# Kernel optimization log

Hardware: AMD Instinct MI355X
Metric: run time of the kernel (lower is better)

The kernel has to match this reference:

```python
import jax, jax.numpy as jnp
import numpy as np

B, T, IN, D = 32, 1024, 1536, 768


def setup_inputs() -> dict:
    key = jax.random.key(0)
    ks = jax.random.split(key, 14)
    s_in = 1.0 / np.sqrt(IN)
    s_d = 1.0 / np.sqrt(D)
    return {
        "x": jax.random.normal(ks[0], (B, T, IN), jnp.float32),
        # fc1/fc2 torch Linear weights stored [out, in]
        "fc1_w": jax.random.normal(ks[1], (IN, IN), jnp.float32) * s_in,
        "fc1_b": jax.random.normal(ks[2], (IN,), jnp.float32) * 0.01,
        "fc2_w": jax.random.normal(ks[3], (D, IN), jnp.float32) * s_in,
        "fc2_b": jax.random.normal(ks[4], (D,), jnp.float32) * 0.01,
        # Unary: Conv1d(D,D,k=1) then Conv1d(D,1,k=1); k=1 conv == per-token linear
        "un_emb_w": jax.random.normal(ks[5], (D, D), jnp.float32) * s_d,
        "un_emb_b": jax.random.normal(ks[6], (D,), jnp.float32) * 0.01,
        "un_red_w": jax.random.normal(ks[7], (1, D), jnp.float32) * s_d,
        "un_red_b": jax.random.normal(ks[8], (1,), jnp.float32) * 0.01,
        # Self Pairwise: x_embedding / y_embedding Conv1d(D,D,k=1)
        "pw_x_w": jax.random.normal(ks[9], (D, D), jnp.float32) * s_d,
        "pw_x_b": jax.random.normal(ks[10], (D,), jnp.float32) * 0.01,
        "pw_y_w": jax.random.normal(ks[11], (D, D), jnp.float32) * s_d,
        "pw_y_b": jax.random.normal(ks[12], (D,), jnp.float32) * 0.01,
        # reduce_potentials: Conv1d(2,1,k=1,bias=False) -> 2 scalars
        "red_w": jax.random.normal(ks[13], (2,), jnp.float32),
    }


def reference(x, fc1_w, fc1_b, fc2_w, fc2_b,
              un_emb_w, un_emb_b, un_red_w, un_red_b,
              pw_x_w, pw_x_b, pw_y_w, pw_y_b, red_w):
    # FGAEmbedder MLP: fc2(relu(fc1(x)))
    h = jax.nn.relu(jnp.einsum('bti,oi->bto', x, fc1_w) + fc1_b)
    u = jnp.einsum('bti,oi->bto', h, fc2_w) + fc2_b            # [B,T,D]

    # Unary potential (dropout is identity at inference)
    e = jax.nn.relu(jnp.einsum('btd,od->bto', u, un_emb_w) + un_emb_b)
    un_pot = (jnp.einsum('btd,od->bto', e, un_red_w) + un_red_b)[..., 0]  # [B,T]

    # Self pairwise: cosine-similarity matrix, marginalized by mean (spatial_dim=None)
    xe = jnp.einsum('btd,od->bto', u, pw_x_w) + pw_x_b
    ye = jnp.einsum('btd,od->bto', u, pw_y_w) + pw_y_b
    xn = xe / jnp.maximum(jnp.linalg.norm(xe, axis=-1, keepdims=True), 1e-12)
    yn = ye / jnp.maximum(jnp.linalg.norm(ye, axis=-1, keepdims=True), 1e-12)
    S = jnp.einsum('btd,bsd->bts', xn, yn)                     # [B,T,T]
    pw_pot = jnp.mean(S, axis=2)                               # [B,T]

    # reduce potentials (Conv1d 2->1 no bias; order: unary then self), softmax attention
    scores = red_w[0] * un_pot + red_w[1] * pw_pot             # [B,T]
    w = jax.nn.softmax(scores, axis=1)
    return jnp.einsum('btd,bt->bd', u, w)                      # [B,D]
```

## Files before the change

kernel.cpp:

```cpp
#include <hip/hip_runtime.h>
#include <stdint.h>

#define MROWS 32768
#define TSEQ  1024
#define BBATCH 32
#define INDIM 1536
#define DDIM  768
#define NCAT  2304

typedef short short8 __attribute__((ext_vector_type(8)));
typedef short short4v __attribute__((ext_vector_type(4)));
typedef float f32x4  __attribute__((ext_vector_type(4)));

__device__ __forceinline__ float b2f(ushort u) {
    union { uint32_t u; float f; } x; x.u = ((uint32_t)u) << 16; return x.f;
}
__device__ __forceinline__ ushort f2b(float f) {
    union { float f; uint32_t u; } x; x.f = f;
    uint32_t r = x.u + 0x7fffu + ((x.u >> 16) & 1u);
    return (ushort)(r >> 16);
}

__device__ __forceinline__ void cvt4(const float* __restrict__ in, ushort* __restrict__ out, int i) {
    float4 v = ((const float4*)in)[i];
    ushort4 o;
    o.x = f2b(v.x); o.y = f2b(v.y); o.z = f2b(v.z); o.w = f2b(v.w);
    ((ushort4*)out)[i] = o;
}

#define C0 12582912
#define C1 13172736
#define C2 13467648
#define C3 13615104
#define C4 13762560
#define C5 13910016
#define C6 13910592
#define C7 13916736
#define C8 13922880
#define C9 13947456
__global__ void cvt_all(const float* __restrict__ x,
                        const float* __restrict__ fc1_w, const float* __restrict__ fc2_w,
                        const float* __restrict__ w3a, const float* __restrict__ w3b,
                        const float* __restrict__ w3c,
                        const float* __restrict__ ba, const float* __restrict__ bb,
                        const float* __restrict__ bc,
                        ushort* __restrict__ X16, ushort* __restrict__ W1,
                        ushort* __restrict__ W2, ushort* __restrict__ W3,
                        float* __restrict__ B3, float* __restrict__ ybar_z,
                        float* __restrict__ out_z, float* __restrict__ stats_z)
{
    int i = blockIdx.x * 256 + threadIdx.x;
    float4 z = {0.f, 0.f, 0.f, 0.f};
    if (i < C0)       cvt4(x, X16, i);
    else if (i < C1)  cvt4(fc1_w, W1, i - C0);
    else if (i < C2)  cvt4(fc2_w, W2, i - C1);
    else if (i < C3)  cvt4(w3a, W3,           i - C2);
    else if (i < C4)  cvt4(w3b, W3 + 589824,  i - C3);
    else if (i < C5)  cvt4(w3c, W3 + 1179648, i - C4);
    else if (i < C6) {
        int j = i - C5;
        const float* src = (j < 192) ? ba : (j < 384) ? bb : bc;
        int off = (j < 192) ? j : (j < 384) ? (j - 192) : (j - 384);
        ((float4*)B3)[j] = ((const float4*)src)[off];
    }
    else if (i < C7)  ((float4*)ybar_z)[i - C6] = z;
    else if (i < C8)  ((float4*)out_z)[i - C7] = z;
    else if (i < C9)  ((float4*)stats_z)[i - C8] = z;
}

__global__ __launch_bounds__(256, 2)
void gemm_bt(const ushort* __restrict__ A, const ushort* __restrict__ Bm,
             const float* __restrict__ bias, ushort* __restrict__ C,
             int M, int N, int K, int relu_ncols,
             const float* __restrict__ urw, float* __restrict__ SE,
             float* __restrict__ SX, float* __restrict__ SY)
{
    __shared__ __align__(16) ushort lA[128 * 64];
    __shared__ __align__(16) ushort lB[128 * 64];

    const int tid  = threadIdx.x;
    const int lane = tid & 63, wave = tid >> 6;
    const int wm = wave & 1, wn = wave >> 1;
    const int quad = lane >> 4, r16 = lane & 15;

    const int ntiles = N >> 7;
    const int xcd = blockIdx.x & 7;
    const int j   = blockIdx.x >> 3;
    const int g   = j / ntiles;
    const int n_t = j - g * ntiles;
    const int m_t = xcd + (g << 3);
    const int m0 = m_t * 128, n0 = n_t * 128;

    const int srow = lane >> 2;
    const int scol = ((lane & 3) ^ ((lane >> 3) & 3)) * 8;
    const int goff = (r16 << 5) + ((quad ^ ((r16 >> 1) & 3)) << 3);

    f32x4 acc[4][4] = {};

    const int kIters = K >> 6;
    for (int kt = 0; kt < kIters; ++kt) {
        const int k0 = kt << 6;
        __syncthreads();
#pragma unroll
        for (int c = 0; c < 4; ++c) {
            int S  = wave * 4 + c;
            int kh = S >> 3, rs = S & 7;
            int row = rs * 16 + srow;
            int kc  = k0 + kh * 32 + scol;
            const ushort* ga = A + (size_t)(m0 + row) * K + kc;
            __builtin_amdgcn_global_load_lds(
                (const __attribute__((address_space(1))) void*)ga,
                (__attribute__((address_space(3))) void*)&lA[S * 512], 16, 0, 0);
            const ushort* gb = Bm + (size_t)(n0 + row) * K + kc;
            __builtin_amdgcn_global_load_lds(
                (const __attribute__((address_space(1))) void*)gb,
                (__attribute__((address_space(3))) void*)&lB[S * 512], 16, 0, 0);
        }
        __syncthreads();

#pragma unroll
        for (int kh = 0; kh < 2; ++kh) {
            short8 af[4], bf[4];
#pragma unroll
            for (int i = 0; i < 4; ++i)
                af[i] = *(const short8*)&lA[kh * 4096 + (wm * 4 + i) * 512 + goff];
#pragma unroll
            for (int j2 = 0; j2 < 4; ++j2)
                bf[j2] = *(const short8*)&lB[kh * 4096 + (wn * 4 + j2) * 512 + goff];
#pragma unroll
            for (int i = 0; i < 4; ++i)
#pragma unroll
                for (int j2 = 0; j2 < 4; ++j2)
                    acc[i][j2] = __builtin_amdgcn_mfma_f32_16x16x32_bf16(af[i], bf[j2], acc[i][j2], 0, 0, 0);
        }
    }

    const bool stats = (urw != nullptr);
    const int sec = n0 / DDIM;
    float st[4][4] = {};
#pragma unroll
    for (int j2 = 0; j2 < 4; ++j2) {
        int gn = n0 + wn * 64 + j2 * 16 + r16;
        float bv = bias[gn];
        bool dorelu = gn < relu_ncols;
        float uw = (stats && sec == 0) ? urw[gn] : 0.f;
#pragma unroll
        for (int i = 0; i < 4; ++i) {
            int gmb = m0 + wm * 64 + i * 16 + quad * 4;
#pragma unroll
            for (int rr = 0; rr < 4; ++rr) {
                float v = acc[i][j2][rr] + bv;
                if (dorelu) v = fmaxf(v, 0.f);
                C[(size_t)(gmb + rr) * N + gn] = f2b(v);
                if (stats) st[i][rr] += (sec == 0) ? v * uw : v * v;
            }
        }
    }
    if (stats) {
#pragma unroll
        for (int i = 0; i < 4; ++i)
#pragma unroll
            for (int rr = 0; rr < 4; ++rr) {
                float v = st[i][rr];
                v += __shfl_xor(v, 1, 64);
                v += __shfl_xor(v, 2, 64);
                v += __shfl_xor(v, 4, 64);
                v += __shfl_xor(v, 8, 64);
                st[i][rr] = v;
            }
        if (r16 == 0) {
            float* dst = (sec == 0) ? SE : (sec == 1) ? SX : SY;
#pragma unroll
            for (int i = 0; i < 4; ++i)
#pragma unroll
                for (int rr = 0; rr < 4; ++rr)
                    atomicAdd(&dst[m0 + wm * 64 + i * 16 + quad * 4 + rr], st[i][rr]);
        }
    }
}

__global__ void ybar_k(const ushort* __restrict__ G3, const float* __restrict__ sy,
                       float* __restrict__ ybar)
{
    int b = blockIdx.x, s0 = blockIdx.y * 32;
    int tid = threadIdx.x;
    __shared__ float sr[32];
    if (tid < 32) {
        float v = sy[b * TSEQ + s0 + tid];
        sr[tid] = (1.0f / TSEQ) / fmaxf(sqrtf(v), 1e-12f);
    }
    __syncthreads();
    float a0 = 0.f, a1 = 0.f, a2 = 0.f;
#pragma unroll 8
    for (int s = 0; s < 32; ++s) {
        const ushort* row = G3 + (size_t)(b * TSEQ + s0 + s) * NCAT + 2 * DDIM;
        float w = sr[s];
        a0 += b2f(row[tid])       * w;
        a1 += b2f(row[tid + 256]) * w;
        a2 += b2f(row[tid + 512]) * w;
    }
    atomicAdd(&ybar[b * DDIM + tid],       a0);
    atomicAdd(&ybar[b * DDIM + tid + 256], a1);
    atomicAdd(&ybar[b * DDIM + tid + 512], a2);
}

__global__ void pw_scores_k(const ushort* __restrict__ G3, const float* __restrict__ ybar,
                            const float* __restrict__ SE, const float* __restrict__ SX,
                            const float* __restrict__ urb, const float* __restrict__ red_w,
                            float* __restrict__ scores)
{
    int wv = threadIdx.x >> 6, lane = threadIdx.x & 63;
    int m = blockIdx.x * 4 + wv;
    int b = m >> 10;
    const ushort* xe = G3 + (size_t)m * NCAT + DDIM;
    const float4* yb = (const float4*)(ybar + b * DDIM);
    float s = 0.f;
#pragma unroll
    for (int c0 = 0; c0 < 3; ++c0) {
        int c = lane + c0 * 64;
        short4v v = *(const short4v*)(xe + c * 4);
        float4 yv = yb[c];
        s += b2f((ushort)v[0]) * yv.x + b2f((ushort)v[1]) * yv.y
           + b2f((ushort)v[2]) * yv.z + b2f((ushort)v[3]) * yv.w;
    }
#pragma unroll
    for (int off = 32; off; off >>= 1) s += __shfl_xor(s, off, 64);
    if (lane == 0) {
        float rnx = 1.f / fmaxf(sqrtf(SX[m]), 1e-12f);
        scores[m] = red_w[0] * (SE[m] + urb[0]) + red_w[1] * (rnx * s);
    }
}

__global__ void out_sm_k(const ushort* __restrict__ U16, const float* __restrict__ scores,
                         float* __restrict__ out)
{
    int b = blockIdx.x, t0 = blockIdx.y * 32;
    int tid = threadIdx.x;
    int lane = tid & 63, wv = tid >> 6;
    __shared__ float red[8];
    __shared__ float sw[32];

    float v[4];
    float lm = -1e30f;
#pragma unroll
    for (int i = 0; i < 4; ++i) {
        v[i] = scores[b * TSEQ + i * 256 + tid];
        lm = fmaxf(lm, v[i]);
    }
#pragma unroll
    for (int off = 32; off; off >>= 1) lm = fmaxf(lm, __shfl_xor(lm, off, 64));
    if (lane == 0) red[wv] = lm;
    __syncthreads();
    float smax = fmaxf(fmaxf(red[0], red[1]), fmaxf(red[2], red[3]));
    float ls = 0.f;
#pragma unroll
    for (int i = 0; i < 4; ++i) ls += expf(v[i] - smax);
#pragma unroll
    for (int off = 32; off; off >>= 1) ls += __shfl_xor(ls, off, 64);
    if (lane == 0) red[4 + wv] = ls;
    __syncthreads();
    float inv = 1.f / (red[4] + red[5] + red[6] + red[7]);

    if (tid < 32) sw[tid] = expf(scores[b * TSEQ + t0 + tid] - smax) * inv;
    __syncthreads();

    float a0 = 0.f, a1 = 0.f, a2 = 0.f;
#pragma unroll 8
    for (int t = 0; t < 32; ++t) {
        const ushort* row = U16 + (size_t)(b * TSEQ + t0 + t) * DDIM;
        float w = sw[t];
        a0 += b2f(row[tid])       * w;
        a1 += b2f(row[tid + 256]) * w;
        a2 += b2f(row[tid + 512]) * w;
    }
    atomicAdd(&out[b * DDIM + tid],       a0);
    atomicAdd(&out[b * DDIM + tid + 256], a1);
    atomicAdd(&out[b * DDIM + tid + 512], a2);
}

static const size_t O_X16   = 0;
static const size_t O_H16   = 100663296;
static const size_t O_G3    = 0;
static const size_t O_U16   = 201326592;
static const size_t O_W1    = 251658240;
static const size_t O_W2    = 256376832;
static const size_t O_W3    = 258736128;
static const size_t O_B3    = 262275072;
static const size_t O_SE    = 262284288;
static const size_t O_SX    = 262415360;
static const size_t O_SY    = 262546432;
static const size_t O_SCORE = 262677504;
static const size_t O_YBAR  = 262939648;

extern "C" void kernel_launch(void* const* d_in, const int* in_sizes, int n_in,
                              void* d_out, int out_size, void* d_ws, size_t ws_size,
                              hipStream_t stream)
{
    const float* x        = (const float*)d_in[0];
    const float* fc1_w    = (const float*)d_in[1];
    const float* fc1_b    = (const float*)d_in[2];
    const float* fc2_w    = (const float*)d_in[3];
    const float* fc2_b    = (const float*)d_in[4];
    const float* un_emb_w = (const float*)d_in[5];
    const float* un_emb_b = (const float*)d_in[6];
    const float* un_red_w = (const float*)d_in[7];
    const float* un_red_b = (const float*)d_in[8];
    const float* pw_x_w   = (const float*)d_in[9];
    const float* pw_x_b   = (const float*)d_in[10];
    const float* pw_y_w   = (const float*)d_in[11];
    const float* pw_y_b   = (const float*)d_in[12];
    const float* red_w    = (const float*)d_in[13];

    char* ws = (char*)d_ws;
    ushort* X16 = (ushort*)(ws + O_X16);
    ushort* H16 = (ushort*)(ws + O_H16);
    ushort* G3  = (ushort*)(ws + O_G3);
    ushort* U16 = (ushort*)(ws + O_U16);
    ushort* W1  = (ushort*)(ws + O_W1);
    ushort* W2  = (ushort*)(ws + O_W2);
    ushort* W3  = (ushort*)(ws + O_W3);
    float*  B3  = (float*)(ws + O_B3);
    float*  SE  = (float*)(ws + O_SE);
    float*  SX  = (float*)(ws + O_SX);
    float*  SY  = (float*)(ws + O_SY);
    float*  SCORES = (float*)(ws + O_SCORE);
    float*  YBAR = (float*)(ws + O_YBAR);

    cvt_all<<<54483, 256, 0, stream>>>(x, fc1_w, fc2_w, un_emb_w, pw_x_w, pw_y_w,
                                       un_emb_b, pw_x_b, pw_y_b,
                                       X16, W1, W2, W3, B3, YBAR, (float*)d_out, SE);

    gemm_bt<<<(MROWS / 128) * (INDIM / 128), 256, 0, stream>>>(
        X16, W1, fc1_b, H16, MROWS, INDIM, INDIM, INDIM,
        nullptr, nullptr, nullptr, nullptr);
    gemm_bt<<<(MROWS / 128) * (DDIM / 128), 256, 0, stream>>>(
        H16, W2, fc2_b, U16, MROWS, DDIM, INDIM, 0,
        nullptr, nullptr, nullptr, nullptr);
    gemm_bt<<<(MROWS / 128) * (NCAT / 128), 256, 0, stream>>>(
        U16, W3, B3, G3, MROWS, NCAT, DDIM, DDIM,
        un_red_w, SE, SX, SY);

    ybar_k<<<dim3(BBATCH, 32), 256, 0, stream>>>(G3, SY, YBAR);
    pw_scores_k<<<MROWS / 4, 256, 0, stream>>>(G3, YBAR, SE, SX, un_red_b, red_w, SCORES);
    out_sm_k<<<dim3(BBATCH, 32), 256, 0, stream>>>(U16, SCORES, (float*)d_out);
}
```

Measured before the change: 717.8 us.

## Fuse fp32-to-bf16 conversion of x into first GEMM and skip unused unary store

Drops the separate pass that converts x to bf16. A new GEMM variant loads fp32 A tiles into registers, converts them to bf16 while staging into LDS, and prefetches the next A tile while the current one is used. This removes a full write and reread of the 100MB bf16 copy of x, at the cost of reading fp32 A, which is twice as many bytes per tile and is reread across the 12 N-tiles. The third GEMM also skips storing the unary embedding section, since only its reduced statistic is consumed afterwards.

```diff
diff --git a/kernel.cpp b/kernel.cpp
--- a/kernel.cpp
+++ b/kernel.cpp
@@ -28,44 +28,142 @@
     ((ushort4*)out)[i] = o;
 }
 
-#define C0 12582912
-#define C1 13172736
-#define C2 13467648
-#define C3 13615104
-#define C4 13762560
-#define C5 13910016
-#define C6 13910592
-#define C7 13916736
-#define C8 13922880
-#define C9 13947456
-__global__ void cvt_all(const float* __restrict__ x,
-                        const float* __restrict__ fc1_w, const float* __restrict__ fc2_w,
+#define C0 589824
+#define C1 884736
+#define C2 1032192
+#define C3 1179648
+#define C4 1327104
+#define C5 1327680
+#define C6 1333824
+#define C7 1339968
+#define C8 1364544
+__global__ void cvt_all(const float* __restrict__ fc1_w, const float* __restrict__ fc2_w,
                         const float* __restrict__ w3a, const float* __restrict__ w3b,
                         const float* __restrict__ w3c,
                         const float* __restrict__ ba, const float* __restrict__ bb,
                         const float* __restrict__ bc,
-                        ushort* __restrict__ X16, ushort* __restrict__ W1,
-                        ushort* __restrict__ W2, ushort* __restrict__ W3,
-                        float* __restrict__ B3, float* __restrict__ ybar_z,
-                        float* __restrict__ out_z, float* __restrict__ stats_z)
+                        ushort* __restrict__ W1, ushort* __restrict__ W2,
+                        ushort* __restrict__ W3, float* __restrict__ B3,
+                        float* __restrict__ ybar_z, float* __restrict__ out_z,
+                        float* __restrict__ stats_z)
 {
     int i = blockIdx.x * 256 + threadIdx.x;
     float4 z = {0.f, 0.f, 0.f, 0.f};
-    if (i < C0)       cvt4(x, X16, i);
-    else if (i < C1)  cvt4(fc1_w, W1, i - C0);
-    else if (i < C2)  cvt4(fc2_w, W2, i - C1);
-    else if (i < C3)  cvt4(w3a, W3,           i - C2);
-    else if (i < C4)  cvt4(w3b, W3 + 589824,  i - C3);
-    else if (i < C5)  cvt4(w3c, W3 + 1179648, i - C4);
-    else if (i < C6) {
-        int j = i - C5;
+    if (i < C0)       cvt4(fc1_w, W1, i);
+    else if (i < C1)  cvt4(fc2_w, W2, i - C0);
+    else if (i < C2)  cvt4(w3a, W3,           i - C1);
+    else if (i < C3)  cvt4(w3b, W3 + 589824,  i - C2);
+    else if (i < C4)  cvt4(w3c, W3 + 1179648, i - C3);
+    else if (i < C5) {
+        int j = i - C4;
         const float* src = (j < 192) ? ba : (j < 384) ? bb : bc;
         int off = (j < 192) ? j : (j < 384) ? (j - 192) : (j - 384);
         ((float4*)B3)[j] = ((const float4*)src)[off];
     }
-    else if (i < C7)  ((float4*)ybar_z)[i - C6] = z;
-    else if (i < C8)  ((float4*)out_z)[i - C7] = z;
-    else if (i < C9)  ((float4*)stats_z)[i - C8] = z;
+    else if (i < C6)  ((float4*)ybar_z)[i - C5] = z;
+    else if (i < C7)  ((float4*)out_z)[i - C6] = z;
+    else if (i < C8)  ((float4*)stats_z)[i - C7] = z;
+}
+
+__global__ __launch_bounds__(256, 2)
+void gemm_a32(const float* __restrict__ A, const ushort* __restrict__ Bm,
+              const float* __restrict__ bias, ushort* __restrict__ C,
+              int M, int N, int K, int relu_ncols)
+{
+    __shared__ __align__(16) ushort lA[128 * 64];
+    __shared__ __align__(16) ushort lB[128 * 64];
+
+    const int tid  = threadIdx.x;
+    const int lane = tid & 63, wave = tid >> 6;
+    const int wm = wave & 1, wn = wave >> 1;
+    const int quad = lane >> 4, r16 = lane & 15;
+
+    const int ntiles = N >> 7;
+    const int xcd = blockIdx.x & 7;
+    const int j   = blockIdx.x >> 3;
+    const int g   = j / ntiles;
+    const int n_t = j - g * ntiles;
+    const int m_t = xcd + (g << 3);
+    const int m0 = m_t * 128, n0 = n_t * 128;
+
+    const int srow = lane >> 2;
+    const int scol = ((lane & 3) ^ ((lane >> 3) & 3)) * 8;
+    const int goff = (r16 << 5) + ((quad ^ ((r16 >> 1) & 3)) << 3);
+
+    float4 pa[4][2];
+#define LOADA(K0)                                                           \
+    {                                                                       \
+        _Pragma("unroll")                                                   \
+        for (int c = 0; c < 4; ++c) {                                       \
+            int S = wave * 4 + c; int kh = S >> 3, rs = S & 7;              \
+            const float* ga = A + (size_t)(m0 + rs * 16 + srow) * K         \
+                              + (K0) + kh * 32 + scol;                      \
+            pa[c][0] = ((const float4*)ga)[0];                              \
+            pa[c][1] = ((const float4*)ga)[1];                              \
+        }                                                                   \
+    }
+
+    LOADA(0);
+    f32x4 acc[4][4] = {};
+
+    const int kIters = K >> 6;
+    for (int kt = 0; kt < kIters; ++kt) {
+        __syncthreads();
+#pragma unroll
+        for (int c = 0; c < 4; ++c) {
+            int S = wave * 4 + c;
+            short8 w;
+            w[0] = (short)f2b(pa[c][0].x); w[1] = (short)f2b(pa[c][0].y);
+            w[2] = (short)f2b(pa[c][0].z); w[3] = (short)f2b(pa[c][0].w);
+            w[4] = (short)f2b(pa[c][1].x); w[5] = (short)f2b(pa[c][1].y);
+            w[6] = (short)f2b(pa[c][1].z); w[7] = (short)f2b(pa[c][1].w);
+            *(short8*)&lA[S * 512 + lane * 8] = w;
+        }
+#pragma unroll
+        for (int c = 0; c < 4; ++c) {
+            int S = wave * 4 + c; int kh = S >> 3, rs = S & 7;
+            const ushort* gb = Bm + (size_t)(n0 + rs * 16 + srow) * K
+                               + (kt << 6) + kh * 32 + scol;
+            __builtin_amdgcn_global_load_lds(
+                (const __attribute__((address_space(1))) void*)gb,
+                (__attribute__((address_space(3))) void*)&lB[S * 512], 16, 0, 0);
+        }
+        if (kt + 1 < kIters) LOADA((kt + 1) << 6);
+        __syncthreads();
+
+#pragma unroll
+        for (int kh = 0; kh < 2; ++kh) {
+            short8 af[4], bf[4];
+#pragma unroll
+            for (int i = 0; i < 4; ++i)
+                af[i] = *(const short8*)&lA[kh * 4096 + (wm * 4 + i) * 512 + goff];
+#pragma unroll
+            for (int j2 = 0; j2 < 4; ++j2)
+                bf[j2] = *(const short8*)&lB[kh * 4096 + (wn * 4 + j2) * 512 + goff];
+#pragma unroll
+            for (int i = 0; i < 4; ++i)
+#pragma unroll
+                for (int j2 = 0; j2 < 4; ++j2)
+                    acc[i][j2] = __builtin_amdgcn_mfma_f32_16x16x32_bf16(af[i], bf[j2], acc[i][j2], 0, 0, 0);
+        }
+    }
+
+#pragma unroll
+    for (int j2 = 0; j2 < 4; ++j2) {
+        int gn = n0 + wn * 64 + j2 * 16 + r16;
+        float bv = bias[gn];
+        bool dorelu = gn < relu_ncols;
+#pragma unroll
+        for (int i = 0; i < 4; ++i) {
+            int gmb = m0 + wm * 64 + i * 16 + quad * 4;
+#pragma unroll
+            for (int rr = 0; rr < 4; ++rr) {
+                float v = acc[i][j2][rr] + bv;
+                if (dorelu) v = fmaxf(v, 0.f);
+                C[(size_t)(gmb + rr) * N + gn] = f2b(v);
+            }
+        }
+    }
 }
 
 __global__ __launch_bounds__(256, 2)
@@ -137,6 +235,7 @@
 
     const bool stats = (urw != nullptr);
     const int sec = n0 / DDIM;
+    const bool dostore = !(stats && sec == 0);
     float st[4][4] = {};
 #pragma unroll
     for (int j2 = 0; j2 < 4; ++j2) {
@@ -151,7 +250,7 @@
             for (int rr = 0; rr < 4; ++rr) {
                 float v = acc[i][j2][rr] + bv;
                 if (dorelu) v = fmaxf(v, 0.f);
-                C[(size_t)(gmb + rr) * N + gn] = f2b(v);
+                if (dostore) C[(size_t)(gmb + rr) * N + gn] = f2b(v);
                 if (stats) st[i][rr] += (sec == 0) ? v * uw : v * v;
             }
         }
@@ -278,7 +377,6 @@
     atomicAdd(&out[b * DDIM + tid + 512], a2);
 }
 
-static const size_t O_X16   = 0;
 static const size_t O_H16   = 100663296;
 static const size_t O_G3    = 0;
 static const size_t O_U16   = 201326592;
@@ -312,7 +410,6 @@
     const float* red_w    = (const float*)d_in[13];
 
     char* ws = (char*)d_ws;
-    ushort* X16 = (ushort*)(ws + O_X16);
     ushort* H16 = (ushort*)(ws + O_H16);
     ushort* G3  = (ushort*)(ws + O_G3);
     ushort* U16 = (ushort*)(ws + O_U16);
@@ -326,13 +423,12 @@
     float*  SCORES = (float*)(ws + O_SCORE);
     float*  YBAR = (float*)(ws + O_YBAR);
 
-    cvt_all<<<54483, 256, 0, stream>>>(x, fc1_w, fc2_w, un_emb_w, pw_x_w, pw_y_w,
-                                       un_emb_b, pw_x_b, pw_y_b,
-                                       X16, W1, W2, W3, B3, YBAR, (float*)d_out, SE);
-
-    gemm_bt<<<(MROWS / 128) * (INDIM / 128), 256, 0, stream>>>(
-        X16, W1, fc1_b, H16, MROWS, INDIM, INDIM, INDIM,
-        nullptr, nullptr, nullptr, nullptr);
+    cvt_all<<<5331, 256, 0, stream>>>(fc1_w, fc2_w, un_emb_w, pw_x_w, pw_y_w,
+                                      un_emb_b, pw_x_b, pw_y_b,
+                                      W1, W2, W3, B3, YBAR, (float*)d_out, SE);
+
+    gemm_a32<<<(MROWS / 128) * (INDIM / 128), 256, 0, stream>>>(
+        x, W1, fc1_b, H16, MROWS, INDIM, INDIM, INDIM);
     gemm_bt<<<(MROWS / 128) * (DDIM / 128), 256, 0, stream>>>(
         H16, W2, fc2_b, U16, MROWS, DDIM, INDIM, 0,
         nullptr, nullptr, nullptr, nullptr);
```

Result: slower. 743.3 us (+3.6%).
